# Performance work log

Measured on AMD Instinct MI355X. Metric: run time of the kernel, lower is better.

Reference implementation:

```python
import jax, jax.numpy as jnp
import numpy as np

L, B, S, D, H, FF, V = 6, 1, 2048, 1024, 16, 4096, 32000
DH = D // H


def _layer_norm(x, g, b, eps=1e-5):
    m = jnp.mean(x, axis=-1, keepdims=True)
    v = jnp.mean((x - m) ** 2, axis=-1, keepdims=True)
    return (x - m) * jax.lax.rsqrt(v + eps) * g + b


def _sinusoidal_pos(seq_len, d, dtype=jnp.float32):
    pos = jnp.arange(seq_len, dtype=dtype)[:, None]
    inv = jnp.power(10000.0, jnp.arange(0, d, 2, dtype=dtype) / d)
    ang = pos / inv  # [S, D/2]
    P = jnp.zeros((seq_len, d), dtype)
    P = P.at[:, 0::2].set(jnp.sin(ang))
    P = P.at[:, 1::2].set(jnp.cos(ang))
    return P


def setup_inputs() -> dict:
    key = jax.random.key(0)
    ks = jax.random.split(key, 8)
    s = 0.02
    return {
        "tokens": jax.random.randint(ks[0], (B, S), 0, V, dtype=jnp.int32),
        "emb": jax.random.normal(ks[1], (V, D), jnp.float32) * s,
        "Wq": jax.random.normal(ks[2], (L, D, D), jnp.float32) * s,
        "Wk": jax.random.normal(ks[3], (L, D, D), jnp.float32) * s,
        "Wv": jax.random.normal(ks[4], (L, D, D), jnp.float32) * s,
        "Wo": jax.random.normal(ks[5], (L, D, D), jnp.float32) * s,
        "ln1_g": jnp.ones((L, D), jnp.float32),
        "ln1_b": jnp.zeros((L, D), jnp.float32),
        "W1": jax.random.normal(ks[6], (L, D, FF), jnp.float32) * s,
        "b1": jnp.zeros((L, FF), jnp.float32),
        "W2": jax.random.normal(ks[7], (L, FF, D), jnp.float32) * s,
        "b2": jnp.zeros((L, D), jnp.float32),
        "ln2_g": jnp.ones((L, D), jnp.float32),
        "ln2_b": jnp.zeros((L, D), jnp.float32),
        "post_g": jnp.ones((D,), jnp.float32),
        "post_b": jnp.zeros((D,), jnp.float32),
    }


def reference(tokens, emb, Wq, Wk, Wv, Wo, ln1_g, ln1_b, W1, b1, W2, b2,
              ln2_g, ln2_b, post_g, post_b):
    dtype = emb.dtype
    b, s = tokens.shape
    h = emb[tokens] + _sinusoidal_pos(s, D, dtype)  # [B, S, D]
    neg = jnp.finfo(dtype).min
    causal = jnp.where(jnp.tril(jnp.ones((s, s), bool)), 0.0, neg).astype(dtype)
    scale = 1.0 / np.sqrt(DH)

    def block(h, p):
        wq, wk, wv, wo, g1, bb1, w1, bm1, w2, bm2, g2, bb2 = p
        q = (h @ wq).reshape(b, s, H, DH)
        k = (h @ wk).reshape(b, s, H, DH)
        v = (h @ wv).reshape(b, s, H, DH)
        scores = jnp.einsum('bqhd,bkhd->bhqk', q, k) * scale + causal
        attn = jax.nn.softmax(scores, axis=-1)
        o = jnp.einsum('bhqk,bkhd->bqhd', attn, v).reshape(b, s, D) @ wo
        h1 = _layer_norm(o + h, g1, bb1)                      # AddNorm1
        m = jnp.maximum(h1 @ w1 + bm1, 0.0) @ w2 + bm2        # MLP
        h2 = _layer_norm(m + h1, g2, bb2)                     # AddNorm2
        return h2, None

    params = (Wq, Wk, Wv, Wo, ln1_g, ln1_b, W1, b1, W2, b2, ln2_g, ln2_b)
    h, _ = jax.lax.scan(block, h, params)
    return _layer_norm(h, post_g, post_b)
```

## Files before the change

kernel.cpp:

```cpp
#include <hip/hip_runtime.h>
#include <hip/hip_bf16.h>

constexpr int S_  = 2048;
constexpr int D_  = 1024;
constexpr int H_  = 16;
constexpr int DH_ = 64;
constexpr int FF_ = 4096;
constexpr int L_  = 6;
constexpr int DQKV_ = 3 * D_;

typedef __attribute__((ext_vector_type(8))) short short8;
typedef __attribute__((ext_vector_type(4))) short s16x4;
typedef __attribute__((ext_vector_type(4))) float f32x4;

__device__ inline short f2bf(float x) {
  __hip_bfloat16 h = __float2bfloat16(x);
  short s; __builtin_memcpy(&s, &h, 2); return s;
}
__device__ inline float bf2f(short s) {
  unsigned int u = ((unsigned int)(unsigned short)s) << 16;
  float f; __builtin_memcpy(&f, &u, 4); return f;
}

__device__ inline void gl2lds16(const void* g, void* l) {
  __builtin_amdgcn_global_load_lds(
      (const __attribute__((address_space(1))) unsigned int*)g,
      (__attribute__((address_space(3))) unsigned int*)l, 16, 0, 0);
}

__device__ inline int swz128(int x) { return x ^ (((x >> 7) & 7) << 4); }

template<bool BIAS, bool RELU, bool OUTBF, bool VTOUT>
__global__ __launch_bounds__(512, 2) void gemm8p(
    const short* __restrict__ A, int lda, long long sAz,
    const short* __restrict__ Bt, int ldb, long long sBz,
    void* __restrict__ Cv, int ldc, long long sCz,
    const float* __restrict__ bias, int K, short* __restrict__ vTout)
{
  constexpr int BM = 256, BN = 128, BK = 64;
  const int m0 = blockIdx.x * BM, n0 = blockIdx.y * BN;
  A  += (long long)blockIdx.z * sAz;
  Bt += (long long)blockIdx.z * sBz;

  __shared__ __align__(16) short lds[2][(BM + BN) * BK];

  const int tid  = threadIdx.x;
  const int lane = tid & 63, wave = tid >> 6;
  const int wr = wave >> 2, wc = wave & 3;
  const int r16 = lane & 15, g = lane >> 4;

  f32x4 acc[8][2];
#pragma unroll
  for (int m = 0; m < 8; m++)
#pragma unroll
    for (int n = 0; n < 2; n++) acc[m][n] = f32x4{0.f, 0.f, 0.f, 0.f};

  const int NT = K / BK;

  auto stage = [&](int buf, int t) {
    char* base = (char*)lds[buf];
#pragma unroll
    for (int r = 0; r < 4; r++) {
      int p = r * 8192 + tid * 16;
      int q = swz128(p);
      int row = q >> 7, kc = (q & 127) >> 1;
      gl2lds16(&A[(size_t)(m0 + row) * lda + t * BK + kc], base + p);
    }
#pragma unroll
    for (int r = 0; r < 2; r++) {
      int p = r * 8192 + tid * 16;
      int q = swz128(p);
      int row = q >> 7, kc = (q & 127) >> 1;
      gl2lds16(&Bt[(size_t)(n0 + row) * ldb + t * BK + kc], base + BM * BK * 2 + p);
    }
  };

  stage(0, 0);
  for (int t = 0; t < NT; t++) {
    __builtin_amdgcn_s_barrier();
    asm volatile("" ::: "memory");
    if (t + 1 < NT) {
      stage((t + 1) & 1, t + 1);
      asm volatile("s_waitcnt vmcnt(6)" ::: "memory");
    } else {
      asm volatile("s_waitcnt vmcnt(0)" ::: "memory");
    }
    __builtin_amdgcn_s_barrier();
    asm volatile("" ::: "memory");

    const char* sa = (const char*)lds[t & 1];
    const char* sb = (const char*)lds[t & 1] + BM * BK * 2;
    const int xo = (r16 & 7) << 4;

    short8 af[8][2], bfr[2][2];
#pragma unroll
    for (int fm = 0; fm < 8; fm++)
#pragma unroll
      for (int kk = 0; kk < 2; kk++) {
        int row = wr * 128 + fm * 16 + r16;
        af[fm][kk] = *(const short8*)(sa + row * 128 + ((kk * 64 + g * 16) ^ xo));
      }
#pragma unroll
    for (int nq = 0; nq < 2; nq++)
#pragma unroll
      for (int kk = 0; kk < 2; kk++) {
        int row = wc * 32 + nq * 16 + r16;
        bfr[nq][kk] = *(const short8*)(sb + row * 128 + ((kk * 64 + g * 16) ^ xo));
      }

    __builtin_amdgcn_s_setprio(1);
#pragma unroll
    for (int fm = 0; fm < 8; fm++)
#pragma unroll
      for (int nq = 0; nq < 2; nq++)
#pragma unroll
        for (int kk = 0; kk < 2; kk++)
          acc[fm][nq] = __builtin_amdgcn_mfma_f32_16x16x32_bf16(
              af[fm][kk], bfr[nq][kk], acc[fm][nq], 0, 0, 0);
    __builtin_amdgcn_s_setprio(0);
  }

  const int rw = g * 4;
#pragma unroll
  for (int am = 0; am < 8; am++) {
#pragma unroll
    for (int an = 0; an < 2; an++) {
      const int rg = m0 + wr * 128 + am * 16 + rw;
      const int cg = n0 + wc * 32 + an * 16 + r16;
      float bv = 0.f;
      if (BIAS) { if (blockIdx.z == 0) bv = bias[cg]; }
      if (VTOUT && cg >= 2 * D_) {
        int hh = (cg - 2 * D_) >> 6, dd = (cg - 2 * D_) & 63;
        s16x4 ov;
#pragma unroll
        for (int j = 0; j < 4; j++) ov[j] = f2bf(acc[am][an][j]);
        *(s16x4*)&vTout[(size_t)hh * DH_ * S_ + (size_t)dd * S_ + rg] = ov;
      } else {
#pragma unroll
        for (int j = 0; j < 4; j++) {
          float v = acc[am][an][j] + bv;
          if (RELU) v = fmaxf(v, 0.f);
          if (OUTBF)
            ((short*)Cv + (long long)blockIdx.z * sCz)[(size_t)(rg + j) * ldc + cg] = f2bf(v);
          else
            ((float*)Cv + (long long)blockIdx.z * sCz)[(size_t)(rg + j) * ldc + cg] = v;
        }
      }
    }
  }
}

__global__ __launch_bounds__(256, 4) void flash_attn(
    const short* __restrict__ qkv, const short* __restrict__ vT,
    short* __restrict__ attno)
{
  const int f = blockIdx.y * gridDim.x + blockIdx.x;
  const int xcd = f & 7, i = f >> 3;
  const int h  = xcd * 2 + (i >> 5);
  const int qb = (31 - (i & 31)) * 64;
  const int tid = threadIdx.x, lane = tid & 63, w = tid >> 6;
  const int r16 = lane & 15, g = lane >> 4, kg = g * 8;

  __shared__ __align__(16) short kv_lds[2][2][64 * 64];
  __shared__ __align__(16) short p_lds[4][16 * 64];

  short8 qreg[2];
  {
    const short* qrow = qkv + (size_t)(qb + w * 16 + r16) * DQKV_ + h * DH_;
    qreg[0] = *(const short8*)&qrow[kg];
    qreg[1] = *(const short8*)&qrow[32 + kg];
  }

  const short* Ksec = qkv + D_ + h * DH_;
  const short* Vsec = vT + (size_t)h * DH_ * S_;

  auto stageKV = [&](int buf, int kv0) {
#pragma unroll
    for (int r = 0; r < 2; r++) {
      int p = r * 4096 + tid * 16;
      int q = swz128(p);
      int row = q >> 7, col = (q & 127) >> 1;
      gl2lds16(&Ksec[(size_t)(kv0 + row) * DQKV_ + col], (char*)kv_lds[buf][0] + p);
    }
#pragma unroll
    for (int r = 0; r < 2; r++) {
      int p = r * 4096 + tid * 16;
      int q = swz128(p);
      int row = q >> 7, col = (q & 127) >> 1;
      gl2lds16(&Vsec[(size_t)row * S_ + kv0 + col], (char*)kv_lds[buf][1] + p);
    }
  };

  f32x4 sacc[4], oacc[4];
#pragma unroll
  for (int m = 0; m < 4; m++) oacc[m] = f32x4{0.f, 0.f, 0.f, 0.f};
  float mrow = -3.0e38f, lrow = 0.f;
  const int qrow_g = qb + w * 16 + r16;
  const int nsteps = qb / 64 + 1;

  stageKV(0, 0);
  int cur = 0;
  for (int s = 0; s < nsteps; s++) {
    __syncthreads();
    if (s + 1 < nsteps) stageKV(cur ^ 1, (s + 1) * 64);

#pragma unroll
    for (int m = 0; m < 4; m++) sacc[m] = f32x4{0.f, 0.f, 0.f, 0.f};
    __builtin_amdgcn_s_setprio(1);
#pragma unroll
    for (int kk = 0; kk < 2; kk++) {
#pragma unroll
      for (int m = 0; m < 4; m++) {
        int lb = (m * 16 + r16) * 128 + (((kk * 32 + kg) * 2) ^ ((r16 & 7) << 4));
        short8 kf = *(const short8*)((const char*)kv_lds[cur][0] + lb);
        sacc[m] = __builtin_amdgcn_mfma_f32_16x16x32_bf16(kf, qreg[kk], sacc[m], 0, 0, 0);
      }
    }
    __builtin_amdgcn_s_setprio(0);

    const int kv0 = s * 64;
    const bool diag = (s == nsteps - 1);
    float mx = mrow;
#pragma unroll
    for (int m = 0; m < 4; m++)
#pragma unroll
      for (int j = 0; j < 4; j++) {
        float x = sacc[m][j] * 0.125f;
        if (diag && (kv0 + m * 16 + g * 4 + j > qrow_g)) x = -3.0e38f;
        sacc[m][j] = x;
        mx = fmaxf(mx, x);
      }
    mx = fmaxf(mx, __shfl_xor(mx, 16));
    mx = fmaxf(mx, __shfl_xor(mx, 32));
    float alpha = __expf(mrow - mx);
    mrow = mx;

    float psum = 0.f;
#pragma unroll
    for (int m = 0; m < 4; m++) {
      s16x4 pk;
#pragma unroll
      for (int j = 0; j < 4; j++) {
        float p = __expf(sacc[m][j] - mx);
        psum += p;
        pk[j] = f2bf(p);
      }
      *(s16x4*)((char*)p_lds[w] + r16 * 128 + (((m * 16 + g * 4) * 2) ^ ((r16 & 7) << 4))) = pk;
    }
    psum += __shfl_xor(psum, 16);
    psum += __shfl_xor(psum, 32);
    lrow = lrow * alpha + psum;

#pragma unroll
    for (int m = 0; m < 4; m++)
#pragma unroll
      for (int j = 0; j < 4; j++) oacc[m][j] *= alpha;

    __builtin_amdgcn_s_setprio(1);
#pragma unroll
    for (int kk = 0; kk < 2; kk++) {
      int pb = r16 * 128 + (((kk * 32 + kg) * 2) ^ ((r16 & 7) << 4));
      short8 pf = *(const short8*)((const char*)p_lds[w] + pb);
#pragma unroll
      for (int m = 0; m < 4; m++) {
        int vb = (m * 16 + r16) * 128 + (((kk * 32 + kg) * 2) ^ ((r16 & 7) << 4));
        short8 vf = *(const short8*)((const char*)kv_lds[cur][1] + vb);
        oacc[m] = __builtin_amdgcn_mfma_f32_16x16x32_bf16(vf, pf, oacc[m], 0, 0, 0);
      }
    }
    __builtin_amdgcn_s_setprio(0);
    cur ^= 1;
  }

  float inv = 1.0f / lrow;
  short* orow = attno + (size_t)qrow_g * D_ + h * DH_;
#pragma unroll
  for (int m = 0; m < 4; m++) {
    s16x4 ov;
#pragma unroll
    for (int j = 0; j < 4; j++) ov[j] = f2bf(oacc[m][j] * inv);
    *(s16x4*)&orow[m * 16 + g * 4] = ov;
  }
}

__global__ __launch_bounds__(256) void weight_prep(
    const float* __restrict__ Wq, const float* __restrict__ Wk,
    const float* __restrict__ Wv, const float* __restrict__ Wo,
    const float* __restrict__ W1, const float* __restrict__ W2,
    short* __restrict__ WqkvT, short* __restrict__ WoT,
    short* __restrict__ W1T, short* __restrict__ W2T)
{
  const int l = blockIdx.x / 3072, r = blockIdx.x % 3072;
  const float* src; short* dst; int K, N, t;
  if (r < 768) {
    int which = r / 256; t = r % 256;
    src = (which == 0 ? Wq : which == 1 ? Wk : Wv) + (size_t)l * D_ * D_;
    dst = WqkvT + (size_t)l * DQKV_ * D_ + (size_t)which * D_ * D_;
    K = D_; N = D_;
  } else if (r < 1024) {
    t = r - 768;
    src = Wo + (size_t)l * D_ * D_; dst = WoT + (size_t)l * D_ * D_;
    K = D_; N = D_;
  } else if (r < 2048) {
    t = r - 1024;
    src = W1 + (size_t)l * D_ * FF_; dst = W1T + (size_t)l * D_ * FF_;
    K = D_; N = FF_;
  } else {
    t = r - 2048;
    src = W2 + (size_t)l * D_ * FF_; dst = W2T + (size_t)l * D_ * FF_;
    K = FF_; N = D_;
  }
  const int xt = N / 64;
  const int n0 = (t % xt) * 64, k0 = (t / xt) * 64;

  __shared__ float tile[64][65];
  int tc = threadIdx.x & 63, tr4 = threadIdx.x >> 6;
#pragma unroll 4
  for (int rr = 0; rr < 64; rr += 4) {
    int rw = rr + tr4;
    tile[rw][tc] = src[(size_t)(k0 + rw) * N + n0 + tc];
  }
  __syncthreads();
#pragma unroll 4
  for (int rr = 0; rr < 64; rr += 4) {
    int rw = rr + tr4;
    dst[(size_t)(n0 + rw) * K + k0 + tc] = f2bf(tile[tc][rw]);
  }
}

__global__ __launch_bounds__(256) void embed_kernel(
    const int* __restrict__ tok, const float* __restrict__ emb,
    float* __restrict__ h, short* __restrict__ hb)
{
  int s = blockIdx.x, t = threadIdx.x;
  int token = tok[s];
  int d0 = t * 4;
  float4 e = *(const float4*)&emb[(size_t)token * D_ + d0];
  float o[4] = {e.x, e.y, e.z, e.w};
#pragma unroll
  for (int c = 0; c < 4; c++) {
    int d = d0 + c;
    float expo = (float)(d & ~1) / (float)D_;
    float inv  = powf(10000.0f, expo);
    float ang  = (float)s / inv;
    o[c] += (d & 1) ? cosf(ang) : sinf(ang);
  }
  float4 ov = {o[0], o[1], o[2], o[3]};
  *(float4*)&h[(size_t)s * D_ + d0] = ov;
  s16x4 sv = {f2bf(o[0]), f2bf(o[1]), f2bf(o[2]), f2bf(o[3])};
  *(s16x4*)&hb[(size_t)s * D_ + d0] = sv;
}

__global__ __launch_bounds__(256) void add_ln_kernel(
    const short* __restrict__ px, int nx, long long xs,
    const float* __restrict__ x32,
    const float* __restrict__ res,
    const float* __restrict__ g, const float* __restrict__ b,
    float* __restrict__ out, short* __restrict__ outb)
{
  int row = blockIdx.x, t = threadIdx.x;
  size_t base = (size_t)row * D_ + t * 4;
  float4 v = {0.f, 0.f, 0.f, 0.f};
  if (px) {
    for (int z = 0; z < nx; z++) {
      s16x4 r = *(const s16x4*)&px[(size_t)z * xs + base];
      v.x += bf2f(r[0]); v.y += bf2f(r[1]); v.z += bf2f(r[2]); v.w += bf2f(r[3]);
    }
  }
  if (x32) {
    float4 r = *(const float4*)&x32[base];
    v.x += r.x; v.y += r.y; v.z += r.z; v.w += r.w;
  }
  if (res) {
    float4 r = *(const float4*)&res[base];
    v.x += r.x; v.y += r.y; v.z += r.z; v.w += r.w;
  }
  float s  = v.x + v.y + v.z + v.w;
  float ss = v.x * v.x + v.y * v.y + v.z * v.z + v.w * v.w;
#pragma unroll
  for (int o = 32; o; o >>= 1) { s += __shfl_xor(s, o); ss += __shfl_xor(ss, o); }
  __shared__ float sh[8];
  int w = t >> 6;
  if ((t & 63) == 0) { sh[w] = s; sh[4 + w] = ss; }
  __syncthreads();
  s  = sh[0] + sh[1] + sh[2] + sh[3];
  ss = sh[4] + sh[5] + sh[6] + sh[7];
  float mean = s * (1.0f / D_);
  float var  = ss * (1.0f / D_) - mean * mean;
  float rinv = rsqrtf(var + 1e-5f);
  float4 gv = *(const float4*)&g[t * 4];
  float4 bv = *(const float4*)&b[t * 4];
  float4 ov;
  ov.x = (v.x - mean) * rinv * gv.x + bv.x;
  ov.y = (v.y - mean) * rinv * gv.y + bv.y;
  ov.z = (v.z - mean) * rinv * gv.z + bv.z;
  ov.w = (v.w - mean) * rinv * gv.w + bv.w;
  *(float4*)&out[base] = ov;
  if (outb) {
    s16x4 sv = {f2bf(ov.x), f2bf(ov.y), f2bf(ov.z), f2bf(ov.w)};
    *(s16x4*)&outb[base] = sv;
  }
}

__global__ void fill_kernel(float* out, int n, float v) {
  int i = blockIdx.x * 256 + threadIdx.x;
  if (i < n) out[i] = v;
}

extern "C" void kernel_launch(void* const* d_in, const int* in_sizes, int n_in,
                              void* d_out, int out_size, void* d_ws, size_t ws_size,
                              hipStream_t stream)
{
  const int*   tokens = (const int*)  d_in[0];
  const float* emb    = (const float*)d_in[1];
  const float* Wq     = (const float*)d_in[2];
  const float* Wk     = (const float*)d_in[3];
  const float* Wv     = (const float*)d_in[4];
  const float* Wo     = (const float*)d_in[5];
  const float* ln1_g  = (const float*)d_in[6];
  const float* ln1_b  = (const float*)d_in[7];
  const float* W1     = (const float*)d_in[8];
  const float* b1     = (const float*)d_in[9];
  const float* W2     = (const float*)d_in[10];
  const float* b2     = (const float*)d_in[11];
  const float* ln2_g  = (const float*)d_in[12];
  const float* ln2_b  = (const float*)d_in[13];
  const float* post_g = (const float*)d_in[14];
  const float* post_b = (const float*)d_in[15];

  size_t off = 0;
  auto alloc = [&](size_t bytes) -> char* {
    char* p = (char*)d_ws + off;
    off = (off + bytes + 255) & ~(size_t)255;
    return p;
  };
  short* WqkvT = (short*)alloc((size_t)L_ * DQKV_ * D_ * 2);
  short* WoT   = (short*)alloc((size_t)L_ * D_ * D_ * 2);
  short* W1T   = (short*)alloc((size_t)L_ * D_ * FF_ * 2);
  short* W2T   = (short*)alloc((size_t)L_ * D_ * FF_ * 2);
  float* h     = (float*)alloc((size_t)S_ * D_ * 4);
  short* hb    = (short*)alloc((size_t)S_ * D_ * 2);
  short* qkv   = (short*)alloc((size_t)S_ * DQKV_ * 2);
  short* vT    = (short*)alloc((size_t)S_ * D_ * 2);
  short* attno = (short*)alloc((size_t)S_ * D_ * 2);
  short* part  = (short*)alloc((size_t)4 * S_ * D_ * 2);
  float* h1    = (float*)alloc((size_t)S_ * D_ * 4);
  short* h1b   = (short*)alloc((size_t)S_ * D_ * 2);
  short* m1    = (short*)alloc((size_t)S_ * FF_ * 2);

  if (off > ws_size) {
    fill_kernel<<<(out_size + 255) / 256, 256, 0, stream>>>(
        (float*)d_out, out_size, (float)(ws_size >> 20));
    return;
  }

  weight_prep<<<L_ * 3072, 256, 0, stream>>>(
      Wq, Wk, Wv, Wo, W1, W2, WqkvT, WoT, W1T, W2T);

  embed_kernel<<<S_, 256, 0, stream>>>(tokens, emb, h, hb);

  for (int l = 0; l < L_; l++) {
    const short* wqkv = WqkvT + (size_t)l * DQKV_ * D_;
    const short* wot  = WoT + (size_t)l * D_ * D_;
    const short* w1t  = W1T + (size_t)l * D_ * FF_;
    const short* w2t  = W2T + (size_t)l * D_ * FF_;

    gemm8p<false, false, true, true>
        <<<dim3(S_ / 256, DQKV_ / 128, 1), 512, 0, stream>>>(
            hb, D_, 0, wqkv, D_, 0, qkv, DQKV_, 0, nullptr, D_, vT);

    flash_attn<<<dim3(S_ / 64, H_), 256, 0, stream>>>(qkv, vT, attno);

    gemm8p<false, false, true, false>
        <<<dim3(S_ / 256, D_ / 128, 4), 512, 0, stream>>>(
            attno, D_, D_ / 4, wot, D_, D_ / 4,
            part, D_, (long long)S_ * D_, nullptr, D_ / 4, nullptr);

    add_ln_kernel<<<S_, 256, 0, stream>>>(part, 4, (long long)S_ * D_, nullptr, h,
                                          ln1_g + (size_t)l * D_,
                                          ln1_b + (size_t)l * D_, h1, h1b);

    gemm8p<true, true, true, false>
        <<<dim3(S_ / 256, FF_ / 128, 1), 512, 0, stream>>>(
            h1b, D_, 0, w1t, D_, 0, m1, FF_, 0, b1 + (size_t)l * FF_, D_, nullptr);

    gemm8p<true, false, true, false>
        <<<dim3(S_ / 256, D_ / 128, 4), 512, 0, stream>>>(
            m1, FF_, FF_ / 4, w2t, FF_, FF_ / 4,
            part, D_, (long long)S_ * D_, b2 + (size_t)l * D_, FF_ / 4, nullptr);

    add_ln_kernel<<<S_, 256, 0, stream>>>(part, 4, (long long)S_ * D_, nullptr, h1,
                                          ln2_g + (size_t)l * D_,
                                          ln2_b + (size_t)l * D_, h, hb);
  }

  add_ln_kernel<<<S_, 256, 0, stream>>>(nullptr, 0, 0, h, nullptr, post_g, post_b,
                                        (float*)d_out, nullptr);
}
```

Measured before the change: 949.4 us.

## Pre-tile and pre-swizzle weights so GEMM B loads are contiguous tile copies

The weight prep kernel now writes each transposed bf16 weight as contiguous 128x64 tiles already in the LDS swizzled order, using vectorized float4 reads and short8 writes. The GEMM B-operand stage then copies each tile linearly from global memory into LDS without per-element swizzle address math. This is meant to cut the cost of weight preparation and make B loads fully coalesced. In exchange the GEMM is tied to this fixed tiled layout through the new kTilesTot/kbz parameters.

```diff
diff --git a/kernel.cpp b/kernel.cpp
--- a/kernel.cpp
+++ b/kernel.cpp
@@ -21,6 +21,10 @@
   unsigned int u = ((unsigned int)(unsigned short)s) << 16;
   float f; __builtin_memcpy(&f, &u, 4); return f;
 }
+__device__ inline unsigned int pack2bf(float a, float b) {
+  return (unsigned int)(unsigned short)f2bf(a) |
+         ((unsigned int)(unsigned short)f2bf(b) << 16);
+}
 
 __device__ inline void gl2lds16(const void* g, void* l) {
   __builtin_amdgcn_global_load_lds(
@@ -33,14 +37,15 @@
 template<bool BIAS, bool RELU, bool OUTBF, bool VTOUT>
 __global__ __launch_bounds__(512, 2) void gemm8p(
     const short* __restrict__ A, int lda, long long sAz,
-    const short* __restrict__ Bt, int ldb, long long sBz,
+    const short* __restrict__ Bt, int kTilesTot, int kbz,
     void* __restrict__ Cv, int ldc, long long sCz,
     const float* __restrict__ bias, int K, short* __restrict__ vTout)
 {
   constexpr int BM = 256, BN = 128, BK = 64;
   const int m0 = blockIdx.x * BM, n0 = blockIdx.y * BN;
-  A  += (long long)blockIdx.z * sAz;
-  Bt += (long long)blockIdx.z * sBz;
+  A += (long long)blockIdx.z * sAz;
+  const short* Bbase = Bt +
+      ((size_t)(n0 >> 7) * kTilesTot + (size_t)blockIdx.z * kbz) * (BN * BK);
 
   __shared__ __align__(16) short lds[2][(BM + BN) * BK];
 
@@ -66,12 +71,11 @@
       int row = q >> 7, kc = (q & 127) >> 1;
       gl2lds16(&A[(size_t)(m0 + row) * lda + t * BK + kc], base + p);
     }
+    const short* btile = Bbase + (size_t)t * (BN * BK);
 #pragma unroll
     for (int r = 0; r < 2; r++) {
       int p = r * 8192 + tid * 16;
-      int q = swz128(p);
-      int row = q >> 7, kc = (q & 127) >> 1;
-      gl2lds16(&Bt[(size_t)(n0 + row) * ldb + t * BK + kc], base + BM * BK * 2 + p);
+      gl2lds16((const char*)btile + p, base + BM * BK * 2 + p);
     }
   };
 
@@ -290,41 +294,59 @@
     short* __restrict__ WqkvT, short* __restrict__ WoT,
     short* __restrict__ W1T, short* __restrict__ W2T)
 {
-  const int l = blockIdx.x / 3072, r = blockIdx.x % 3072;
-  const float* src; short* dst; int K, N, t;
-  if (r < 768) {
-    int which = r / 256; t = r % 256;
-    src = (which == 0 ? Wq : which == 1 ? Wk : Wv) + (size_t)l * D_ * D_;
-    dst = WqkvT + (size_t)l * DQKV_ * D_ + (size_t)which * D_ * D_;
-    K = D_; N = D_;
+  const int l = blockIdx.y, r = blockIdx.x;
+  const float* src; short* dstb; int N, t, ks;
+  if (r < 384) {
+    int which = r >> 7; t = r & 127;
+    src  = (which == 0 ? Wq : which == 1 ? Wk : Wv) + (size_t)l * D_ * D_;
+    dstb = WqkvT + (size_t)l * DQKV_ * D_ + (size_t)which * D_ * D_;
+    N = D_; ks = 4;
+  } else if (r < 512) {
+    t = r - 384;
+    src = Wo + (size_t)l * D_ * D_; dstb = WoT + (size_t)l * D_ * D_;
+    N = D_; ks = 4;
   } else if (r < 1024) {
-    t = r - 768;
-    src = Wo + (size_t)l * D_ * D_; dst = WoT + (size_t)l * D_ * D_;
-    K = D_; N = D_;
-  } else if (r < 2048) {
+    t = r - 512;
+    src = W1 + (size_t)l * D_ * FF_; dstb = W1T + (size_t)l * D_ * FF_;
+    N = FF_; ks = 4;
+  } else {
     t = r - 1024;
-    src = W1 + (size_t)l * D_ * FF_; dst = W1T + (size_t)l * D_ * FF_;
-    K = D_; N = FF_;
-  } else {
-    t = r - 2048;
-    src = W2 + (size_t)l * D_ * FF_; dst = W2T + (size_t)l * D_ * FF_;
-    K = FF_; N = D_;
-  }
-  const int xt = N / 64;
-  const int n0 = (t % xt) * 64, k0 = (t / xt) * 64;
-
-  __shared__ float tile[64][65];
-  int tc = threadIdx.x & 63, tr4 = threadIdx.x >> 6;
-#pragma unroll 4
-  for (int rr = 0; rr < 64; rr += 4) {
-    int rw = rr + tr4;
-    tile[rw][tc] = src[(size_t)(k0 + rw) * N + n0 + tc];
+    src = W2 + (size_t)l * D_ * FF_; dstb = W2T + (size_t)l * D_ * FF_;
+    N = D_; ks = 6;
+  }
+  const int kT = 1 << ks;
+  const int nt = t >> ks, kt = t & (kT - 1);
+  const int n0 = nt * 128, k0 = kt * 64;
+  short* out = dstb + ((size_t)nt * kT + kt) * (128 * 64);
+
+  __shared__ short tile[64][130];
+  const int tid = threadIdx.x;
+
+  {
+    const int kr = tid >> 5;
+    const int c4 = (tid & 31) * 4;
+    const float* sp = &src[(size_t)(k0 + kr) * N + n0 + c4];
+    float4 f[8];
+#pragma unroll
+    for (int i = 0; i < 8; i++) f[i] = *(const float4*)(sp + (size_t)i * 8 * N);
+#pragma unroll
+    for (int i = 0; i < 8; i++) {
+      unsigned int* pw = (unsigned int*)&tile[kr + i * 8][c4];
+      pw[0] = pack2bf(f[i].x, f[i].y);
+      pw[1] = pack2bf(f[i].z, f[i].w);
+    }
   }
   __syncthreads();
-#pragma unroll 4
-  for (int rr = 0; rr < 64; rr += 4) {
-    int rw = rr + tr4;
-    dst[(size_t)(n0 + rw) * K + k0 + tc] = f2bf(tile[tc][rw]);
+
+#pragma unroll
+  for (int rr = 0; rr < 4; rr++) {
+    const int p = (rr * 256 + tid) * 16;
+    const int q = swz128(p);
+    const int n = q >> 7, k = (q & 127) >> 1;
+    short8 o;
+#pragma unroll
+    for (int j = 0; j < 8; j++) o[j] = tile[k + j][n];
+    *(short8*)((char*)out + p) = o;
   }
 }
 
@@ -454,7 +476,7 @@
     return;
   }
 
-  weight_prep<<<L_ * 3072, 256, 0, stream>>>(
+  weight_prep<<<dim3(1536, L_), 256, 0, stream>>>(
       Wq, Wk, Wv, Wo, W1, W2, WqkvT, WoT, W1T, W2T);
 
   embed_kernel<<<S_, 256, 0, stream>>>(tokens, emb, h, hb);
@@ -467,13 +489,13 @@
 
     gemm8p<false, false, true, true>
         <<<dim3(S_ / 256, DQKV_ / 128, 1), 512, 0, stream>>>(
-            hb, D_, 0, wqkv, D_, 0, qkv, DQKV_, 0, nullptr, D_, vT);
+            hb, D_, 0, wqkv, 16, 0, qkv, DQKV_, 0, nullptr, D_, vT);
 
     flash_attn<<<dim3(S_ / 64, H_), 256, 0, stream>>>(qkv, vT, attno);
 
     gemm8p<false, false, true, false>
         <<<dim3(S_ / 256, D_ / 128, 4), 512, 0, stream>>>(
-            attno, D_, D_ / 4, wot, D_, D_ / 4,
+            attno, D_, D_ / 4, wot, 16, 4,
             part, D_, (long long)S_ * D_, nullptr, D_ / 4, nullptr);
 
     add_ln_kernel<<<S_, 256, 0, stream>>>(part, 4, (long long)S_ * D_, nullptr, h,
@@ -482,11 +504,11 @@
 
     gemm8p<true, true, true, false>
         <<<dim3(S_ / 256, FF_ / 128, 1), 512, 0, stream>>>(
-            h1b, D_, 0, w1t, D_, 0, m1, FF_, 0, b1 + (size_t)l * FF_, D_, nullptr);
+            h1b, D_, 0, w1t, 16, 0, m1, FF_, 0, b1 + (size_t)l * FF_, D_, nullptr);
 
     gemm8p<true, false, true, false>
         <<<dim3(S_ / 256, D_ / 128, 4), 512, 0, stream>>>(
-            m1, FF_, FF_ / 4, w2t, FF_, FF_ / 4,
+            m1, FF_, FF_ / 4, w2t, 64, 16,
             part, D_, (long long)S_ * D_, b2 + (size_t)l * D_, FF_ / 4, nullptr);
 
     add_ln_kernel<<<S_, 256, 0, stream>>>(part, 4, (long long)S_ * D_, nullptr, h1,
```

Result: no change. 943.4 us (-0.6%).

## Fuse weight fp32-to-bf16 transpose into GEMM B-tile loading, drop weight_prep

Applied to the files above, without the earlier changes.

Removes the separate weight_prep kernel that transposed and converted all fp32 weights to bf16. Each GEMM now reads fp32 weight columns directly into registers, converts them to bf16 and writes the swizzled B tile into LDS, double-buffered in registers across K steps. This removes a large pre-pass and its extra global traffic. In exchange every GEMM reads fp32 weights (twice the bytes of bf16) with strided per-thread loads, adds register pressure, and adds a conversion and LDS store step to the main loop.

```diff
diff --git a/kernel.cpp b/kernel.cpp
--- a/kernel.cpp
+++ b/kernel.cpp
@@ -33,14 +33,25 @@
 template<bool BIAS, bool RELU, bool OUTBF, bool VTOUT>
 __global__ __launch_bounds__(512, 2) void gemm8p(
     const short* __restrict__ A, int lda, long long sAz,
-    const short* __restrict__ Bt, int ldb, long long sBz,
+    const float* __restrict__ Bq, const float* __restrict__ Bk,
+    const float* __restrict__ Bv, int ldb, long long sBzRows,
     void* __restrict__ Cv, int ldc, long long sCz,
     const float* __restrict__ bias, int K, short* __restrict__ vTout)
 {
   constexpr int BM = 256, BN = 128, BK = 64;
   const int m0 = blockIdx.x * BM, n0 = blockIdx.y * BN;
-  A  += (long long)blockIdx.z * sAz;
-  Bt += (long long)blockIdx.z * sBz;
+  A += (long long)blockIdx.z * sAz;
+
+  const float* bsrc;
+  int ncol;
+  if (VTOUT) {
+    int which = n0 >> 10;
+    bsrc = (which == 0) ? Bq : (which == 1) ? Bk : Bv;
+    ncol = n0 & 1023;
+  } else {
+    bsrc = Bq;
+    ncol = n0;
+  }
 
   __shared__ __align__(16) short lds[2][(BM + BN) * BK];
 
@@ -49,6 +60,11 @@
   const int wr = wave >> 2, wc = wave & 3;
   const int r16 = lane & 15, g = lane >> 4;
 
+  const int nloc = tid & 127;
+  const int kb   = (tid >> 7) * 16;
+  const long long zrow = (long long)blockIdx.z * sBzRows;
+  const float* bcol = bsrc + (size_t)(zrow + kb) * ldb + (ncol + nloc);
+
   f32x4 acc[8][2];
 #pragma unroll
   for (int m = 0; m < 8; m++)
@@ -57,68 +73,90 @@
 
   const int NT = K / BK;
 
-  auto stage = [&](int buf, int t) {
-    char* base = (char*)lds[buf];
+  float bA[16], bB[16];
+
+#pragma unroll
+  for (int j = 0; j < 16; j++) bA[j] = bcol[(size_t)j * ldb];
+  {
+    char* nbase = (char*)lds[0];
 #pragma unroll
     for (int r = 0; r < 4; r++) {
       int p = r * 8192 + tid * 16;
       int q = swz128(p);
       int row = q >> 7, kc = (q & 127) >> 1;
-      gl2lds16(&A[(size_t)(m0 + row) * lda + t * BK + kc], base + p);
-    }
-#pragma unroll
-    for (int r = 0; r < 2; r++) {
-      int p = r * 8192 + tid * 16;
-      int q = swz128(p);
-      int row = q >> 7, kc = (q & 127) >> 1;
-      gl2lds16(&Bt[(size_t)(n0 + row) * ldb + t * BK + kc], base + BM * BK * 2 + p);
-    }
-  };
-
-  stage(0, 0);
-  for (int t = 0; t < NT; t++) {
-    __builtin_amdgcn_s_barrier();
-    asm volatile("" ::: "memory");
-    if (t + 1 < NT) {
-      stage((t + 1) & 1, t + 1);
-      asm volatile("s_waitcnt vmcnt(6)" ::: "memory");
-    } else {
-      asm volatile("s_waitcnt vmcnt(0)" ::: "memory");
-    }
-    __builtin_amdgcn_s_barrier();
-    asm volatile("" ::: "memory");
-
-    const char* sa = (const char*)lds[t & 1];
-    const char* sb = (const char*)lds[t & 1] + BM * BK * 2;
-    const int xo = (r16 & 7) << 4;
-
-    short8 af[8][2], bfr[2][2];
-#pragma unroll
-    for (int fm = 0; fm < 8; fm++)
-#pragma unroll
-      for (int kk = 0; kk < 2; kk++) {
-        int row = wr * 128 + fm * 16 + r16;
-        af[fm][kk] = *(const short8*)(sa + row * 128 + ((kk * 64 + g * 16) ^ xo));
-      }
-#pragma unroll
-    for (int nq = 0; nq < 2; nq++)
-#pragma unroll
-      for (int kk = 0; kk < 2; kk++) {
-        int row = wc * 32 + nq * 16 + r16;
-        bfr[nq][kk] = *(const short8*)(sb + row * 128 + ((kk * 64 + g * 16) ^ xo));
-      }
-
-    __builtin_amdgcn_s_setprio(1);
-#pragma unroll
-    for (int fm = 0; fm < 8; fm++)
-#pragma unroll
-      for (int nq = 0; nq < 2; nq++)
-#pragma unroll
-        for (int kk = 0; kk < 2; kk++)
-          acc[fm][nq] = __builtin_amdgcn_mfma_f32_16x16x32_bf16(
-              af[fm][kk], bfr[nq][kk], acc[fm][nq], 0, 0, 0);
-    __builtin_amdgcn_s_setprio(0);
-  }
+      gl2lds16(&A[(size_t)(m0 + row) * lda + kc], nbase + p);
+    }
+  }
+
+#define GBODY(BCUR, BNXT, TT, PF)                                              \
+  {                                                                            \
+    const int tt = (TT);                                                       \
+    char* base = (char*)lds[tt & 1];                                           \
+    char* sbB  = base + BM * BK * 2;                                           \
+    if (PF) {                                                                  \
+      const float* bp = bcol + (size_t)(tt + 1) * BK * ldb;                    \
+      _Pragma("unroll")                                                        \
+      for (int j = 0; j < 16; j++) BNXT[j] = bp[(size_t)j * ldb];              \
+      char* nbase = (char*)lds[(tt + 1) & 1];                                  \
+      _Pragma("unroll")                                                        \
+      for (int r = 0; r < 4; r++) {                                            \
+        int p = r * 8192 + tid * 16;                                           \
+        int q = swz128(p);                                                     \
+        int row = q >> 7, kc = (q & 127) >> 1;                                 \
+        gl2lds16(&A[(size_t)(m0 + row) * lda + (tt + 1) * BK + kc], nbase + p);\
+      }                                                                        \
+      asm volatile("s_waitcnt vmcnt(20)" ::: "memory");    \
+    } else {                                                                   \
+      asm volatile("s_waitcnt vmcnt(0)" ::: "memory");     \
+    }                                                                          \
+                      \
+    _Pragma("unroll")                                                          \
+    for (int i = 0; i < 2; i++) {                                              \
+      short8 sv;                                                               \
+      _Pragma("unroll")                                                        \
+      for (int jj = 0; jj < 8; jj++) sv[jj] = f2bf(BCUR[i * 8 + jj]);          \
+      int q = nloc * 128 + (kb + i * 8) * 2;                                   \
+      *(short8*)(sbB + swz128(q)) = sv;                                        \
+    }                                                                          \
+    asm volatile("s_waitcnt lgkmcnt(0)" ::: "memory");                         \
+    __builtin_amdgcn_s_barrier();             \
+    asm volatile("" ::: "memory");                                             \
+    const char* sa = base;                                                     \
+    const int xo = (r16 & 7) << 4;                                             \
+    short8 af[8][2], bfr[2][2];                                                \
+    _Pragma("unroll")                                                          \
+    for (int fm = 0; fm < 8; fm++)                                             \
+      _Pragma("unroll")                                                        \
+      for (int kk = 0; kk < 2; kk++) {                                         \
+        int row = wr * 128 + fm * 16 + r16;                                    \
+        af[fm][kk] = *(const short8*)(sa + row * 128 + ((kk * 64 + g * 16) ^ xo)); \
+      }                                                                        \
+    _Pragma("unroll")                                                          \
+    for (int nq = 0; nq < 2; nq++)                                             \
+      _Pragma("unroll")                                                        \
+      for (int kk = 0; kk < 2; kk++) {                                         \
+        int row = wc * 32 + nq * 16 + r16;                                     \
+        bfr[nq][kk] = *(const short8*)(sbB + row * 128 + ((kk * 64 + g * 16) ^ xo)); \
+      }                                                                        \
+    __builtin_amdgcn_s_setprio(1);                                             \
+    _Pragma("unroll")                                                          \
+    for (int fm = 0; fm < 8; fm++)                                             \
+      _Pragma("unroll")                                                        \
+      for (int nq = 0; nq < 2; nq++)                                           \
+        _Pragma("unroll")                                                      \
+        for (int kk = 0; kk < 2; kk++)                                         \
+          acc[fm][nq] = __builtin_amdgcn_mfma_f32_16x16x32_bf16(               \
+              af[fm][kk], bfr[nq][kk], acc[fm][nq], 0, 0, 0);                  \
+    __builtin_amdgcn_s_setprio(0);                                             \
+    __builtin_amdgcn_s_barrier();        \
+    asm volatile("" ::: "memory");                                             \
+  }
+
+  for (int t = 0; t < NT; t += 2) {
+    GBODY(bA, bB, t, true)
+    GBODY(bB, bA, t + 1, (t + 2 < NT))
+  }
+#undef GBODY
 
   const int rw = g * 4;
 #pragma unroll
@@ -280,51 +318,6 @@
 #pragma unroll
     for (int j = 0; j < 4; j++) ov[j] = f2bf(oacc[m][j] * inv);
     *(s16x4*)&orow[m * 16 + g * 4] = ov;
-  }
-}
-
-__global__ __launch_bounds__(256) void weight_prep(
-    const float* __restrict__ Wq, const float* __restrict__ Wk,
-    const float* __restrict__ Wv, const float* __restrict__ Wo,
-    const float* __restrict__ W1, const float* __restrict__ W2,
-    short* __restrict__ WqkvT, short* __restrict__ WoT,
-    short* __restrict__ W1T, short* __restrict__ W2T)
-{
-  const int l = blockIdx.x / 3072, r = blockIdx.x % 3072;
-  const float* src; short* dst; int K, N, t;
-  if (r < 768) {
-    int which = r / 256; t = r % 256;
-    src = (which == 0 ? Wq : which == 1 ? Wk : Wv) + (size_t)l * D_ * D_;
-    dst = WqkvT + (size_t)l * DQKV_ * D_ + (size_t)which * D_ * D_;
-    K = D_; N = D_;
-  } else if (r < 1024) {
-    t = r - 768;
-    src = Wo + (size_t)l * D_ * D_; dst = WoT + (size_t)l * D_ * D_;
-    K = D_; N = D_;
-  } else if (r < 2048) {
-    t = r - 1024;
-    src = W1 + (size_t)l * D_ * FF_; dst = W1T + (size_t)l * D_ * FF_;
-    K = D_; N = FF_;
-  } else {
-    t = r - 2048;
-    src = W2 + (size_t)l * D_ * FF_; dst = W2T + (size_t)l * D_ * FF_;
-    K = FF_; N = D_;
-  }
-  const int xt = N / 64;
-  const int n0 = (t % xt) * 64, k0 = (t / xt) * 64;
-
-  __shared__ float tile[64][65];
-  int tc = threadIdx.x & 63, tr4 = threadIdx.x >> 6;
-#pragma unroll 4
-  for (int rr = 0; rr < 64; rr += 4) {
-    int rw = rr + tr4;
-    tile[rw][tc] = src[(size_t)(k0 + rw) * N + n0 + tc];
-  }
-  __syncthreads();
-#pragma unroll 4
-  for (int rr = 0; rr < 64; rr += 4) {
-    int rw = rr + tr4;
-    dst[(size_t)(n0 + rw) * K + k0 + tc] = f2bf(tile[tc][rw]);
   }
 }
 
@@ -434,10 +427,6 @@
     off = (off + bytes + 255) & ~(size_t)255;
     return p;
   };
-  short* WqkvT = (short*)alloc((size_t)L_ * DQKV_ * D_ * 2);
-  short* WoT   = (short*)alloc((size_t)L_ * D_ * D_ * 2);
-  short* W1T   = (short*)alloc((size_t)L_ * D_ * FF_ * 2);
-  short* W2T   = (short*)alloc((size_t)L_ * D_ * FF_ * 2);
   float* h     = (float*)alloc((size_t)S_ * D_ * 4);
   short* hb    = (short*)alloc((size_t)S_ * D_ * 2);
   short* qkv   = (short*)alloc((size_t)S_ * DQKV_ * 2);
@@ -454,26 +443,26 @@
     return;
   }
 
-  weight_prep<<<L_ * 3072, 256, 0, stream>>>(
-      Wq, Wk, Wv, Wo, W1, W2, WqkvT, WoT, W1T, W2T);
-
   embed_kernel<<<S_, 256, 0, stream>>>(tokens, emb, h, hb);
 
   for (int l = 0; l < L_; l++) {
-    const short* wqkv = WqkvT + (size_t)l * DQKV_ * D_;
-    const short* wot  = WoT + (size_t)l * D_ * D_;
-    const short* w1t  = W1T + (size_t)l * D_ * FF_;
-    const short* w2t  = W2T + (size_t)l * D_ * FF_;
+    const float* wq_l = Wq + (size_t)l * D_ * D_;
+    const float* wk_l = Wk + (size_t)l * D_ * D_;
+    const float* wv_l = Wv + (size_t)l * D_ * D_;
+    const float* wo_l = Wo + (size_t)l * D_ * D_;
+    const float* w1_l = W1 + (size_t)l * D_ * FF_;
+    const float* w2_l = W2 + (size_t)l * D_ * FF_;
 
     gemm8p<false, false, true, true>
         <<<dim3(S_ / 256, DQKV_ / 128, 1), 512, 0, stream>>>(
-            hb, D_, 0, wqkv, D_, 0, qkv, DQKV_, 0, nullptr, D_, vT);
+            hb, D_, 0, wq_l, wk_l, wv_l, D_, 0,
+            qkv, DQKV_, 0, nullptr, D_, vT);
 
     flash_attn<<<dim3(S_ / 64, H_), 256, 0, stream>>>(qkv, vT, attno);
 
     gemm8p<false, false, true, false>
         <<<dim3(S_ / 256, D_ / 128, 4), 512, 0, stream>>>(
-            attno, D_, D_ / 4, wot, D_, D_ / 4,
+            attno, D_, D_ / 4, wo_l, wo_l, wo_l, D_, D_ / 4,
             part, D_, (long long)S_ * D_, nullptr, D_ / 4, nullptr);
 
     add_ln_kernel<<<S_, 256, 0, stream>>>(part, 4, (long long)S_ * D_, nullptr, h,
@@ -482,11 +471,12 @@
 
     gemm8p<true, true, true, false>
         <<<dim3(S_ / 256, FF_ / 128, 1), 512, 0, stream>>>(
-            h1b, D_, 0, w1t, D_, 0, m1, FF_, 0, b1 + (size_t)l * FF_, D_, nullptr);
+            h1b, D_, 0, w1_l, w1_l, w1_l, FF_, 0,
+            m1, FF_, 0, b1 + (size_t)l * FF_, D_, nullptr);
 
     gemm8p<true, false, true, false>
         <<<dim3(S_ / 256, D_ / 128, 4), 512, 0, stream>>>(
-            m1, FF_, FF_ / 4, w2t, FF_, FF_ / 4,
+            m1, FF_, FF_ / 4, w2_l, w2_l, w2_l, D_, FF_ / 4,
             part, D_, (long long)S_ * D_, b2 + (size_t)l * D_, FF_ / 4, nullptr);
 
     add_ln_kernel<<<S_, 256, 0, stream>>>(part, 4, (long long)S_ * D_, nullptr, h1,
```

Measured after the change: 1.121 ms. +18.1%, slower.
